# Performance work log

Hardware: AMD Instinct MI355X
Metric: run time of the kernel (lower is better)

Reference implementation:

```python
import jax, jax.numpy as jnp
import numpy as np

NUM_HEADS = 64          # also the positional-embedding size (quirk of the module)
DIM_IN, DIM_K, DIM_V = 512, 512, 64
BATCH, SEQ = 4, 1024


def setup_inputs() -> dict:
    key = jax.random.key(0)
    ks = jax.random.split(key, 7)
    s = 0.05  # weight init scale
    return {
        "x":  jax.random.normal(ks[0], (BATCH, SEQ, DIM_IN), jnp.float32),
        "Wq": jax.random.normal(ks[1], (DIM_IN, DIM_K), jnp.float32) * s,
        "bq": jax.random.normal(ks[2], (DIM_K,), jnp.float32) * s,
        "Wk": jax.random.normal(ks[3], (DIM_IN, DIM_K), jnp.float32) * s,
        "bk": jax.random.normal(ks[4], (DIM_K,), jnp.float32) * s,
        "Wv": jax.random.normal(ks[5], (DIM_IN, DIM_V), jnp.float32) * s,
        "bv": jax.random.normal(ks[6], (DIM_V,), jnp.float32) * s,
    }


def _position_embedding(n, position_size):
    # matches Position_Enbedding: cos block then sin block along feature dim
    half = position_size // 2
    pos_j = 1.0 / jnp.power(10000.0, 2.0 * jnp.arange(half, dtype=jnp.float32) / position_size)
    pos_ij = jnp.arange(n, dtype=jnp.float32)[:, None] * pos_j[None, :]   # [n, half]
    return jnp.concatenate([jnp.cos(pos_ij), jnp.sin(pos_ij)], axis=1)    # [n, position_size]


def reference(x, Wq, bq, Wk, bk, Wv, bv):
    B, n, _ = x.shape
    nh = NUM_HEADS
    dk = DIM_K // nh   # 8
    dv = DIM_V // nh   # 1
    # fused linear + ReLU, then split heads: [B, nh, n, d]
    q = jax.nn.relu(x @ Wq + bq).reshape(B, n, nh, dk).transpose(0, 2, 1, 3)
    k = jax.nn.relu(x @ Wk + bk).reshape(B, n, nh, dk).transpose(0, 2, 1, 3)
    v = jax.nn.relu(x @ Wv + bv).reshape(B, n, nh, dv).transpose(0, 2, 1, 3)
    scale = 1.0 / np.sqrt(dk).astype(np.float32)
    dist = jax.nn.softmax(jnp.einsum('bhqd,bhkd->bhqk', q, k) * scale, axis=-1)
    att = jnp.einsum('bhqk,bhkd->bhqd', dist, v)            # [B, nh, n, dv]
    att = att.transpose(0, 2, 1, 3).reshape(B, n, DIM_V)    # [B, n, dim_v]
    pe = _position_embedding(n, nh)                          # [n, nh] == [n, dim_v]
    return att + pe[None, :, :]
```

## Files before the change

### kernel.cpp

```cpp
#include <hip/hip_runtime.h>
#include <math.h>

#define BATCH 4
#define SEQ   1024
#define DIN   512
#define DKQ   512
#define DV    64
#define NH    64

typedef __attribute__((ext_vector_type(8))) short short8v;
typedef __attribute__((ext_vector_type(4))) float float4v;
typedef __attribute__((ext_vector_type(4))) unsigned int uint4v;

__device__ __forceinline__ void split_bf16(float f, unsigned short& hi, unsigned short& lo) {
    unsigned int u = __float_as_uint(f);
    hi = (unsigned short)(u >> 16);
    float l = f - __uint_as_float(u & 0xFFFF0000u);
    lo = (unsigned short)(__float_as_uint(l) >> 16);
}
__device__ __forceinline__ unsigned short f32_to_bf16_rne(float f) {
    unsigned int u = __float_as_uint(f);
    u += 0x7FFFu + ((u >> 16) & 1u);
    return (unsigned short)(u >> 16);
}
__device__ __forceinline__ float bf16_bits_to_f32(unsigned short s) {
    return __uint_as_float((unsigned int)s << 16);
}

__device__ __forceinline__ void gll16(const unsigned short* g, unsigned short* l) {
    __builtin_amdgcn_global_load_lds(
        (const __attribute__((address_space(1))) unsigned int*)(g),
        (__attribute__((address_space(3))) unsigned int*)(l),
        16, 0, 0);
}

__global__ __launch_bounds__(256)
void prepack(const float* __restrict__ x,
             const float* __restrict__ Wq, const float* __restrict__ Wk,
             const float* __restrict__ Wv,
             unsigned short* __restrict__ WhiQ, unsigned short* __restrict__ WloQ,
             unsigned short* __restrict__ WhiK, unsigned short* __restrict__ WloK,
             unsigned short* __restrict__ WhiV, unsigned short* __restrict__ WloV,
             unsigned short* __restrict__ Xhi, unsigned short* __restrict__ Xlo,
             unsigned int* __restrict__ obuf)
{
    const int z = blockIdx.z;
    const int tx = threadIdx.x, ty = threadIdx.y;
    if (z == 3) {
        const int t = ty * 32 + tx;
        const int bid = blockIdx.y * 16 + blockIdx.x;
        if (bid == 0 && t < 8)
            obuf[t] = (t < 4) ? 0x3F803F80u : 0u;
        #pragma unroll
        for (int j = 0; j < 4; ++j) {
            const int i = ((bid * 4 + j) * 256 + t) * 8;
            float4 a0 = *(const float4*)&x[i];
            float4 a1 = *(const float4*)&x[i + 4];
            float av[8] = {a0.x, a0.y, a0.z, a0.w, a1.x, a1.y, a1.z, a1.w};
            short8v h, l;
            #pragma unroll
            for (int jj = 0; jj < 8; ++jj) {
                unsigned short hh, ll; split_bf16(av[jj], hh, ll);
                h[jj] = (short)hh; l[jj] = (short)ll;
            }
            *(short8v*)&Xhi[i] = h;
            *(short8v*)&Xlo[i] = l;
        }
        return;
    }
    const int N = (z == 2) ? DV : DKQ;
    if (z == 2 && blockIdx.x >= 2) return;
    const float* __restrict__ W = (z == 0) ? Wq : (z == 1) ? Wk : Wv;
    unsigned short* __restrict__ Whi = (z == 0) ? WhiQ : (z == 1) ? WhiK : WhiV;
    unsigned short* __restrict__ Wlo = (z == 0) ? WloQ : (z == 1) ? WloK : WloV;

    __shared__ float tile[32][33];
    const int n0 = blockIdx.x * 32, k0 = blockIdx.y * 32;
    #pragma unroll
    for (int i = 0; i < 32; i += 8)
        tile[ty + i][tx] = W[(size_t)(k0 + ty + i) * N + n0 + tx];
    __syncthreads();
    #pragma unroll
    for (int i = 0; i < 32; i += 8) {
        unsigned short h, l; split_bf16(tile[tx][ty + i], h, l);
        Whi[(size_t)(n0 + ty + i) * DIN + k0 + tx] = h;
        Wlo[(size_t)(n0 + ty + i) * DIN + k0 + tx] = l;
    }
}

__global__ __launch_bounds__(512)
void proj_kernel(const unsigned short* __restrict__ Xhi,
                 const unsigned short* __restrict__ Xlo,
                 const unsigned short* __restrict__ WhiQ, const unsigned short* __restrict__ WloQ,
                 const float* __restrict__ bq,
                 const unsigned short* __restrict__ WhiK, const unsigned short* __restrict__ WloK,
                 const float* __restrict__ bk,
                 const unsigned short* __restrict__ WhiV, const unsigned short* __restrict__ WloV,
                 const float* __restrict__ bv,
                 unsigned short* __restrict__ Qpk, unsigned short* __restrict__ Kpk,
                 unsigned int* __restrict__ Vsh, unsigned int* __restrict__ Vsl)
{
    const int z = blockIdx.z;
    if (z == 2 && blockIdx.x != 0) return;
    const unsigned short* __restrict__ Whi = (z == 0) ? WhiQ : (z == 1) ? WhiK : WhiV;
    const unsigned short* __restrict__ Wlo = (z == 0) ? WloQ : (z == 1) ? WloK : WloV;
    const float* __restrict__ bias = (z == 0) ? bq : (z == 1) ? bk : bv;

    __shared__ unsigned short LDS[2][16384];

    const int t = threadIdx.x;
    const int wave = t >> 6, lane = t & 63;
    const int cl = lane & 15, g2 = lane >> 4;
    const int bm  = blockIdx.y * 128;
    const int cbb = (z == 2) ? 0 : blockIdx.x * 128;
    const int wr = wave >> 2, wc = wave & 3;
    const int NF = (z == 2) ? 1 : 2;

    const unsigned short* sAh = Xhi + (size_t)(bm + wave * 16 + cl) * DIN + g2 * 8;
    const unsigned short* sAl = Xlo + (size_t)(bm + wave * 16 + cl) * DIN + g2 * 8;
    const bool bvalid = (z != 2) || (wave < 4);
    const size_t bro = (size_t)(cbb + wave * 16 + cl) * DIN + g2 * 8;
    const unsigned short* sBh = Whi + (bvalid ? bro : 0);
    const unsigned short* sBl = Wlo + (bvalid ? bro : 0);

    auto stage = [&](int step, int bufIdx) {
        unsigned short* L = &LDS[bufIdx][0];
        const int kofs = step * 32;
        gll16(sAh + kofs, L + (wave) * 512);
        gll16(sAl + kofs, L + (wave + 8) * 512);
        if (bvalid) {
            gll16(sBh + kofs, L + (wave + 16) * 512);
            gll16(sBl + kofs, L + (wave + 24) * 512);
        }
    };

    float4v acc[4][2];
    #pragma unroll
    for (int i = 0; i < 4; ++i)
        #pragma unroll
        for (int j = 0; j < 2; ++j)
            acc[i][j] = (float4v){0.f, 0.f, 0.f, 0.f};

    stage(0, 0);
    __syncthreads();

    #pragma unroll
    for (int ks = 0; ks < 16; ++ks) {
        const int cur = ks & 1;
        if (ks < 15) stage(ks + 1, cur ^ 1);

        const unsigned short* L = &LDS[cur][0];
        short8v af_h[4], af_l[4], bf_h[2], bf_l[2];
        #pragma unroll
        for (int mt = 0; mt < 4; ++mt) {
            af_h[mt] = *(const short8v*)(L + (wr * 4 + mt) * 512 + lane * 8);
            af_l[mt] = *(const short8v*)(L + (8 + wr * 4 + mt) * 512 + lane * 8);
        }
        #pragma unroll
        for (int nf = 0; nf < 2; ++nf) {
            if (nf < NF) {
                bf_h[nf] = *(const short8v*)(L + (16 + wc * NF + nf) * 512 + lane * 8);
                bf_l[nf] = *(const short8v*)(L + (24 + wc * NF + nf) * 512 + lane * 8);
            }
        }
        #pragma unroll
        for (int mt = 0; mt < 4; ++mt)
            #pragma unroll
            for (int nf = 0; nf < 2; ++nf) {
                if (nf >= NF) continue;
                acc[mt][nf] = __builtin_amdgcn_mfma_f32_16x16x32_bf16(af_h[mt], bf_h[nf], acc[mt][nf], 0, 0, 0);
                acc[mt][nf] = __builtin_amdgcn_mfma_f32_16x16x32_bf16(af_l[mt], bf_h[nf], acc[mt][nf], 0, 0, 0);
                acc[mt][nf] = __builtin_amdgcn_mfma_f32_16x16x32_bf16(af_h[mt], bf_l[nf], acc[mt][nf], 0, 0, 0);
            }
        __syncthreads();
    }

    const float cc = 0.35355339059327373f * 1.4426950408889634f;
    if (z == 2) {
        const int n = wc * 16 + cl;
        const float bn = bias[n];
        #pragma unroll
        for (int mt = 0; mt < 4; ++mt) {
            const int row0 = bm + wr * 64 + mt * 16 + g2 * 4;
            const int bb = row0 >> 10, s0 = row0 & 1023;
            const int idx0 = (s0 >> 5) * 16 + ((s0 >> 2) & 3) * 4 + ((s0 >> 4) & 1) * 2;
            float vv[4]; unsigned short hh[4], ll[4];
            #pragma unroll
            for (int r = 0; r < 4; ++r) {
                vv[r] = fmaxf(acc[mt][0][r] + bn, 0.0f);
                hh[r] = f32_to_bf16_rne(vv[r]);
                ll[r] = f32_to_bf16_rne(vv[r] - bf16_bits_to_f32(hh[r]));
            }
            const size_t base = (size_t)((bb << 6) + n) * 512 + idx0;
            Vsh[base]     = (unsigned int)hh[0] | ((unsigned int)hh[1] << 16);
            Vsh[base + 1] = (unsigned int)hh[2] | ((unsigned int)hh[3] << 16);
            Vsl[base]     = (unsigned int)ll[0] | ((unsigned int)ll[1] << 16);
            Vsl[base + 1] = (unsigned int)ll[2] | ((unsigned int)ll[3] << 16);
        }
    } else {
        unsigned short* __restrict__ dst = (z == 0) ? Qpk : Kpk;
        unsigned short* Lb = &LDS[0][0] + wave * 512;
        const int hd = cl >> 3, d = cl & 7;
        const int lhd = lane >> 5, lrem = lane & 31;
        const int ls = lrem >> 1, lhalf = lrem & 1;
        #pragma unroll
        for (int mt = 0; mt < 4; ++mt) {
            const int row0 = bm + wr * 64 + mt * 16;
            const int bb = row0 >> 10, s0 = row0 & 1023;
            #pragma unroll
            for (int nf = 0; nf < 2; ++nf) {
                const int nbase = cbb + wc * 32 + nf * 16;
                const float bn = bias[nbase + cl];
                #pragma unroll
                for (int r = 0; r < 4; ++r) {
                    float val = fmaxf(acc[mt][nf][r] + bn, 0.0f);
                    if (z == 0) val *= cc;
                    unsigned short hi = f32_to_bf16_rne(val);
                    unsigned short lo = f32_to_bf16_rne(val - bf16_bits_to_f32(hi));
                    const int sl = g2 * 4 + r;
                    Lb[hd * 256 + sl * 16 + d]     = hi;
                    Lb[hd * 256 + sl * 16 + 8 + d] = lo;
                }
                short8v vv = *(const short8v*)(Lb + lhd * 256 + ls * 16 + lhalf * 8);
                const int h = (nbase >> 3) + lhd;
                const size_t off = ((size_t)((bb << 6) + h) * SEQ + s0 + ls) * 16 + lhalf * 8;
                *(short8v*)(dst + off) = vv;
            }
        }
    }
}

__global__ __launch_bounds__(256, 4)
void attn_kernel(const unsigned short* __restrict__ Qpk,
                 const unsigned short* __restrict__ Kpk,
                 const unsigned int* __restrict__ Vsh,
                 const unsigned int* __restrict__ Vsl,
                 const unsigned int* __restrict__ obuf,
                 float2* __restrict__ part)
{
    const int bh = blockIdx.x;
    const int yb = blockIdx.y;
    const int qhalf = yb >> 2;
    const int kq = yb & 3;
    const int t = threadIdx.x;
    const int wave = t >> 6, lane = t & 63;
    const int g = lane >> 4, cl = lane & 15;

    const unsigned short* __restrict__ qb = Qpk + (size_t)bh * SEQ * 16;
    const unsigned short* __restrict__ kb = Kpk + (size_t)bh * SEQ * 16;

    const int q0 = qhalf * 512 + wave * 128;

    short8v bq[8];
    #pragma unroll
    for (int qt = 0; qt < 8; ++qt) {
        if (g == 3) { short8v zz = {0,0,0,0,0,0,0,0}; bq[qt] = zz; }
        else bq[qt] = *(const short8v*)(qb + (size_t)(q0 + qt * 16 + cl) * 16 + ((g == 1) ? 8 : 0));
    }

    const int koff = (g >> 1) * 8;
    const unsigned short* kp = kb + kq * 4096 + cl * 16 + koff;

    const unsigned int* ap;
    int astr;
    {
        const size_t vb = (size_t)bh * 512 + kq * 128 + g * 4;
        if (cl == 0)      { ap = Vsh + vb; astr = 16; }
        else if (cl == 2) { ap = Vsl + vb; astr = 16; }
        else if (cl == 1) { ap = obuf;     astr = 0;  }
        else              { ap = obuf + 4; astr = 0;  }
    }

    const float4v c0 = {0.f, 0.f, 0.f, 0.f};
    float4v acc[8];
    #pragma unroll
    for (int qt = 0; qt < 8; ++qt) acc[qt] = c0;

    short8v k0c = *(const short8v*)kp;
    short8v k1c = *(const short8v*)(kp + 256);
    uint4v  auc = *(const uint4v*)ap;

    #pragma unroll
    for (int ss = 0; ss < 8; ++ss) {
        short8v k0n, k1n; uint4v aun;
        if (ss < 7) {
            k0n = *(const short8v*)(kp + 512);
            k1n = *(const short8v*)(kp + 768);
            aun = *(const uint4v*)(ap + astr);
        }
        kp += 512; ap += astr;
        const short8v af = __builtin_bit_cast(short8v, auc);
        #pragma unroll
        for (int qt = 0; qt < 8; ++qt) {
            float4v s0 = __builtin_amdgcn_mfma_f32_16x16x32_bf16(k0c, bq[qt], c0, 0, 0, 0);
            float4v s1 = __builtin_amdgcn_mfma_f32_16x16x32_bf16(k1c, bq[qt], c0, 0, 0, 0);
            float p00 = __builtin_amdgcn_exp2f(s0[0]);
            float p01 = __builtin_amdgcn_exp2f(s0[1]);
            float p02 = __builtin_amdgcn_exp2f(s0[2]);
            float p03 = __builtin_amdgcn_exp2f(s0[3]);
            float p10 = __builtin_amdgcn_exp2f(s1[0]);
            float p11 = __builtin_amdgcn_exp2f(s1[1]);
            float p12 = __builtin_amdgcn_exp2f(s1[2]);
            float p13 = __builtin_amdgcn_exp2f(s1[3]);
            unsigned int pk0 = __builtin_amdgcn_perm(__float_as_uint(p01), __float_as_uint(p00), 0x07060302u);
            unsigned int pk1 = __builtin_amdgcn_perm(__float_as_uint(p03), __float_as_uint(p02), 0x07060302u);
            unsigned int pk2 = __builtin_amdgcn_perm(__float_as_uint(p11), __float_as_uint(p10), 0x07060302u);
            unsigned int pk3 = __builtin_amdgcn_perm(__float_as_uint(p13), __float_as_uint(p12), 0x07060302u);
            uint4v pu = {pk0, pk1, pk2, pk3};
            acc[qt] = __builtin_amdgcn_mfma_f32_16x16x32_bf16(af, __builtin_bit_cast(short8v, pu), acc[qt], 0, 0, 0);
        }
        if (ss < 7) { k0c = k0n; k1c = k1n; auc = aun; }
    }

    if (g == 0) {
        #pragma unroll
        for (int qt = 0; qt < 8; ++qt) {
            const int row = q0 + qt * 16 + cl;
            float2 pr;
            pr.x = acc[qt][0] + acc[qt][2];
            pr.y = acc[qt][1];
            part[(size_t)(kq * 256 + bh) * SEQ + row] = pr;
        }
    }
}

__global__ __launch_bounds__(256)
void merge_kernel(const float2* __restrict__ part, float* __restrict__ out)
{
    const int tid = blockIdx.x * 256 + threadIdx.x;
    const int h = tid & 63;
    const int q = (tid >> 6) & 1023;
    const int b = tid >> 16;
    const int bh = (b << 6) + h;
    float num = 0.f, den = 0.f;
    #pragma unroll
    for (int kq = 0; kq < 4; ++kq) {
        float2 p = part[(size_t)(kq * 256 + bh) * SEQ + q];
        num += p.x; den += p.y;
    }
    const float fr = __builtin_amdgcn_exp2f((float)(h & 31) * -0.4152410118609203f);
    const float pe = (h < 32) ? cosf((float)q * fr) : sinf((float)q * fr);
    out[tid] = num / den + pe;
}

extern "C" void kernel_launch(void* const* d_in, const int* in_sizes, int n_in,
                              void* d_out, int out_size, void* d_ws, size_t ws_size,
                              hipStream_t stream)
{
    const float* x  = (const float*)d_in[0];
    const float* Wq = (const float*)d_in[1];
    const float* bq = (const float*)d_in[2];
    const float* Wk = (const float*)d_in[3];
    const float* bk = (const float*)d_in[4];
    const float* Wv = (const float*)d_in[5];
    const float* bv = (const float*)d_in[6];
    float* out = (float*)d_out;

    unsigned short* Qpk = (unsigned short*)d_ws;
    unsigned short* Kpk = Qpk + (size_t)BATCH * NH * SEQ * 16;
    unsigned int* Vsh = (unsigned int*)(Kpk + (size_t)BATCH * NH * SEQ * 16);
    unsigned int* Vsl = Vsh + (size_t)BATCH * NH * (SEQ / 2);
    unsigned int* obuf = Vsl + (size_t)BATCH * NH * (SEQ / 2);
    unsigned short* Xhi = (unsigned short*)(obuf + 64);
    unsigned short* Xlo = Xhi + (size_t)BATCH * SEQ * DIN;
    float2* part = (float2*)Xhi;
    unsigned short* WhiQ = Xlo + (size_t)BATCH * SEQ * DIN;
    unsigned short* WloQ = WhiQ + (size_t)DIN * DKQ;
    unsigned short* WhiK = WloQ + (size_t)DIN * DKQ;
    unsigned short* WloK = WhiK + (size_t)DIN * DKQ;
    unsigned short* WhiV = WloK + (size_t)DIN * DKQ;
    unsigned short* WloV = WhiV + (size_t)DIN * DV;

    prepack<<<dim3(16, 16, 4), dim3(32, 8), 0, stream>>>(
        x, Wq, Wk, Wv, WhiQ, WloQ, WhiK, WloK, WhiV, WloV, Xhi, Xlo, obuf);
    proj_kernel<<<dim3(4, 32, 3), 512, 0, stream>>>(
        Xhi, Xlo, WhiQ, WloQ, bq, WhiK, WloK, bk, WhiV, WloV, bv, Qpk, Kpk, Vsh, Vsl);
    attn_kernel<<<dim3(256, 8), 256, 0, stream>>>(Qpk, Kpk, Vsh, Vsl, obuf, part);
    merge_kernel<<<dim3((BATCH * SEQ * DV) / 256), 256, 0, stream>>>(part, out);
}
```

Baseline: 82.27 us.

## Shrink projection tiles to 64x64 and use triple-buffered LDS with vmcnt waits

```diff
diff --git a/kernel.cpp b/kernel.cpp
--- a/kernel.cpp
+++ b/kernel.cpp
@@ -33,6 +33,8 @@
         (__attribute__((address_space(3))) unsigned int*)(l),
         16, 0, 0);
 }
+__device__ __forceinline__ void waitv4() { asm volatile("s_waitcnt vmcnt(4)" ::: "memory"); }
+__device__ __forceinline__ void waitv0() { asm volatile("s_waitcnt vmcnt(0)" ::: "memory"); }
 
 __global__ __launch_bounds__(256)
 void prepack(const float* __restrict__ x,
@@ -88,7 +90,7 @@
     }
 }
 
-__global__ __launch_bounds__(512)
+__global__ __launch_bounds__(256)
 void proj_kernel(const unsigned short* __restrict__ Xhi,
                  const unsigned short* __restrict__ Xlo,
                  const unsigned short* __restrict__ WhiQ, const unsigned short* __restrict__ WloQ,
@@ -106,96 +108,98 @@
     const unsigned short* __restrict__ Wlo = (z == 0) ? WloQ : (z == 1) ? WloK : WloV;
     const float* __restrict__ bias = (z == 0) ? bq : (z == 1) ? bk : bv;
 
-    __shared__ unsigned short LDS[2][16384];
+    __shared__ unsigned short LDS[3][8192];
 
     const int t = threadIdx.x;
     const int wave = t >> 6, lane = t & 63;
     const int cl = lane & 15, g2 = lane >> 4;
-    const int bm  = blockIdx.y * 128;
-    const int cbb = (z == 2) ? 0 : blockIdx.x * 128;
-    const int wr = wave >> 2, wc = wave & 3;
-    const int NF = (z == 2) ? 1 : 2;
+    const int bm  = blockIdx.y * 64;
+    const int cbb = (z == 2) ? 0 : blockIdx.x * 64;
+    const int wr = wave >> 1, wc = wave & 1;
 
     const unsigned short* sAh = Xhi + (size_t)(bm + wave * 16 + cl) * DIN + g2 * 8;
     const unsigned short* sAl = Xlo + (size_t)(bm + wave * 16 + cl) * DIN + g2 * 8;
-    const bool bvalid = (z != 2) || (wave < 4);
-    const size_t bro = (size_t)(cbb + wave * 16 + cl) * DIN + g2 * 8;
-    const unsigned short* sBh = Whi + (bvalid ? bro : 0);
-    const unsigned short* sBl = Wlo + (bvalid ? bro : 0);
+    const unsigned short* sBh = Whi + (size_t)(cbb + wave * 16 + cl) * DIN + g2 * 8;
+    const unsigned short* sBl = Wlo + (size_t)(cbb + wave * 16 + cl) * DIN + g2 * 8;
 
     auto stage = [&](int step, int bufIdx) {
         unsigned short* L = &LDS[bufIdx][0];
         const int kofs = step * 32;
-        gll16(sAh + kofs, L + (wave) * 512);
-        gll16(sAl + kofs, L + (wave + 8) * 512);
-        if (bvalid) {
-            gll16(sBh + kofs, L + (wave + 16) * 512);
-            gll16(sBl + kofs, L + (wave + 24) * 512);
-        }
+        gll16(sAh + kofs, L + (wave)      * 512);
+        gll16(sAl + kofs, L + (4 + wave)  * 512);
+        gll16(sBh + kofs, L + (8 + wave)  * 512);
+        gll16(sBl + kofs, L + (12 + wave) * 512);
     };
 
-    float4v acc[4][2];
-    #pragma unroll
-    for (int i = 0; i < 4; ++i)
+    float4v acc[2][2];
+    #pragma unroll
+    for (int i = 0; i < 2; ++i)
         #pragma unroll
         for (int j = 0; j < 2; ++j)
             acc[i][j] = (float4v){0.f, 0.f, 0.f, 0.f};
 
     stage(0, 0);
-    __syncthreads();
+    stage(1, 1);
+    waitv4();
+    __builtin_amdgcn_s_barrier();
+    __builtin_amdgcn_sched_barrier(0);
 
     #pragma unroll
     for (int ks = 0; ks < 16; ++ks) {
-        const int cur = ks & 1;
-        if (ks < 15) stage(ks + 1, cur ^ 1);
-
-        const unsigned short* L = &LDS[cur][0];
-        short8v af_h[4], af_l[4], bf_h[2], bf_l[2];
-        #pragma unroll
-        for (int mt = 0; mt < 4; ++mt) {
-            af_h[mt] = *(const short8v*)(L + (wr * 4 + mt) * 512 + lane * 8);
-            af_l[mt] = *(const short8v*)(L + (8 + wr * 4 + mt) * 512 + lane * 8);
+        if (ks + 2 < 16) stage(ks + 2, (ks + 2) % 3);
+
+        const unsigned short* L = &LDS[ks % 3][0];
+        short8v af_h[2], af_l[2], bf_h[2], bf_l[2];
+        #pragma unroll
+        for (int mt = 0; mt < 2; ++mt) {
+            const int st = wr * 2 + mt;
+            af_h[mt] = *(const short8v*)(L + st * 512 + lane * 8);
+            af_l[mt] = *(const short8v*)(L + (4 + st) * 512 + lane * 8);
         }
         #pragma unroll
         for (int nf = 0; nf < 2; ++nf) {
-            if (nf < NF) {
-                bf_h[nf] = *(const short8v*)(L + (16 + wc * NF + nf) * 512 + lane * 8);
-                bf_l[nf] = *(const short8v*)(L + (24 + wc * NF + nf) * 512 + lane * 8);
-            }
-        }
-        #pragma unroll
-        for (int mt = 0; mt < 4; ++mt)
+            const int st = wc * 2 + nf;
+            bf_h[nf] = *(const short8v*)(L + (8 + st) * 512 + lane * 8);
+            bf_l[nf] = *(const short8v*)(L + (12 + st) * 512 + lane * 8);
+        }
+        #pragma unroll
+        for (int mt = 0; mt < 2; ++mt)
             #pragma unroll
             for (int nf = 0; nf < 2; ++nf) {
-                if (nf >= NF) continue;
                 acc[mt][nf] = __builtin_amdgcn_mfma_f32_16x16x32_bf16(af_h[mt], bf_h[nf], acc[mt][nf], 0, 0, 0);
                 acc[mt][nf] = __builtin_amdgcn_mfma_f32_16x16x32_bf16(af_l[mt], bf_h[nf], acc[mt][nf], 0, 0, 0);
                 acc[mt][nf] = __builtin_amdgcn_mfma_f32_16x16x32_bf16(af_h[mt], bf_l[nf], acc[mt][nf], 0, 0, 0);
             }
-        __syncthreads();
+
+        if (ks < 14) waitv4(); else waitv0();
+        __builtin_amdgcn_s_barrier();
+        __builtin_amdgcn_sched_barrier(0);
     }
 
     const float cc = 0.35355339059327373f * 1.4426950408889634f;
     if (z == 2) {
-        const int n = wc * 16 + cl;
-        const float bn = bias[n];
-        #pragma unroll
-        for (int mt = 0; mt < 4; ++mt) {
-            const int row0 = bm + wr * 64 + mt * 16 + g2 * 4;
-            const int bb = row0 >> 10, s0 = row0 & 1023;
-            const int idx0 = (s0 >> 5) * 16 + ((s0 >> 2) & 3) * 4 + ((s0 >> 4) & 1) * 2;
-            float vv[4]; unsigned short hh[4], ll[4];
+        #pragma unroll
+        for (int nf = 0; nf < 2; ++nf) {
+            const int n = wc * 32 + nf * 16 + cl;
+            const float bn = bias[n];
             #pragma unroll
-            for (int r = 0; r < 4; ++r) {
-                vv[r] = fmaxf(acc[mt][0][r] + bn, 0.0f);
-                hh[r] = f32_to_bf16_rne(vv[r]);
-                ll[r] = f32_to_bf16_rne(vv[r] - bf16_bits_to_f32(hh[r]));
+            for (int mt = 0; mt < 2; ++mt) {
+                const int row0 = bm + wr * 32 + mt * 16 + g2 * 4;
+                const int bb = row0 >> 10, s0 = row0 & 1023;
+                const int idx0 = (s0 >> 5) * 16 + ((s0 >> 2) & 3) * 4 + ((s0 >> 4) & 1) * 2;
+                float vv[4]; unsigned short hh[4], ll[4];
+                #pragma unroll
+                for (int r = 0; r < 4; ++r) {
+                    vv[r] = fmaxf(acc[mt][nf][r] + bn, 0.0f);
+                    hh[r] = f32_to_bf16_rne(vv[r]);
+                    ll[r] = f32_to_bf16_rne(vv[r] - bf16_bits_to_f32(hh[r]));
+                }
+                const size_t base = (size_t)((bb << 6) + n) * 512 + idx0;
+                Vsh[base]     = (unsigned int)hh[0] | ((unsigned int)hh[1] << 16);
+                Vsh[base + 1] = (unsigned int)hh[2] | ((unsigned int)hh[3] << 16);
+                Vsl[base]     = (unsigned int)ll[0] | ((unsigned int)ll[1] << 16);
+                Vsl[base + 1] = (unsigned int)ll[2] | ((unsigned int)ll[3] << 16);
             }
-            const size_t base = (size_t)((bb << 6) + n) * 512 + idx0;
-            Vsh[base]     = (unsigned int)hh[0] | ((unsigned int)hh[1] << 16);
-            Vsh[base + 1] = (unsigned int)hh[2] | ((unsigned int)hh[3] << 16);
-            Vsl[base]     = (unsigned int)ll[0] | ((unsigned int)ll[1] << 16);
-            Vsl[base + 1] = (unsigned int)ll[2] | ((unsigned int)ll[3] << 16);
         }
     } else {
         unsigned short* __restrict__ dst = (z == 0) ? Qpk : Kpk;
@@ -204,8 +208,8 @@
         const int lhd = lane >> 5, lrem = lane & 31;
         const int ls = lrem >> 1, lhalf = lrem & 1;
         #pragma unroll
-        for (int mt = 0; mt < 4; ++mt) {
-            const int row0 = bm + wr * 64 + mt * 16;
+        for (int mt = 0; mt < 2; ++mt) {
+            const int row0 = bm + wr * 32 + mt * 16;
             const int bb = row0 >> 10, s0 = row0 & 1023;
             #pragma unroll
             for (int nf = 0; nf < 2; ++nf) {
@@ -373,7 +377,7 @@
 
     prepack<<<dim3(16, 16, 4), dim3(32, 8), 0, stream>>>(
         x, Wq, Wk, Wv, WhiQ, WloQ, WhiK, WloK, WhiV, WloV, Xhi, Xlo, obuf);
-    proj_kernel<<<dim3(4, 32, 3), 512, 0, stream>>>(
+    proj_kernel<<<dim3(8, 64, 3), 256, 0, stream>>>(
         Xhi, Xlo, WhiQ, WloQ, bq, WhiK, WloK, bk, WhiV, WloV, bv, Qpk, Kpk, Vsh, Vsl);
     attn_kernel<<<dim3(256, 8), 256, 0, stream>>>(Qpk, Kpk, Vsh, Vsl, obuf, part);
     merge_kernel<<<dim3((BATCH * SEQ * DV) / 256), 256, 0, stream>>>(part, out);
```

Result: slower. 100.0 us (+21.6%).
